# Optimization experiments

Measured on AMD Instinct MI355X. Metric: run time of the kernel, lower is better.

Reference implementation:

```python
import jax, jax.numpy as jnp
import numpy as np

DIM = 512; NHEAD = 8; DHEAD = 64; INNER = NHEAD * DHEAD
CTX = 1024; NOCT = int(np.ceil(np.log2(CTX))) + 1  # 11
B = 8; SEQ = 256; MEM = 768


def positional_encoding(ctx, num_oct):
    # matches Attention.positional_encoding on coords=arange(ctx).view(ctx,1),
    # start_octave = 1 - num_oct
    coords = jnp.arange(ctx, dtype=jnp.float32)[:, None, None]        # (ctx,1,1)
    octaves = jnp.arange(1 - num_oct, 1, dtype=jnp.float32)           # (num_oct,)
    mult = (2.0 ** octaves) * np.pi
    scaled = (coords * mult).reshape(ctx, num_oct)                    # (ctx, num_oct)
    return jnp.concatenate([jnp.sin(scaled), jnp.cos(scaled)], axis=-1)  # (ctx, 2*num_oct)


def get_shifts(mem, seq, ctx):
    coords = jnp.arange(mem + seq - 1, -1, -1) - (seq - 1)            # (mem+seq,)
    shifts = coords[None, :] + jnp.arange(seq)[:, None]               # (seq, mem+seq)
    oob = (shifts < 0) | (shifts > ctx - 1)
    bias = jnp.where(oob, -jnp.inf, 0.0).astype(jnp.float32)
    return jnp.clip(shifts, 0, ctx - 1), bias


def setup_inputs() -> dict:
    key = jax.random.key(0)
    ks = jax.random.split(key, 8)
    s = 0.02
    return {
        "x": jax.random.normal(ks[0], (B, SEQ, DIM), jnp.float32),
        "memory": jax.random.normal(ks[1], (B, MEM, DIM), jnp.float32),
        "W_qkv": jax.random.normal(ks[2], (DIM, 3 * INNER), jnp.float32) * s,
        "W_rel": jax.random.normal(ks[3], (2 * NOCT, INNER), jnp.float32) * s,
        "W_out": jax.random.normal(ks[4], (INNER, DIM), jnp.float32) * s,
        "b_out": jnp.zeros((DIM,), jnp.float32),
        "u_emb": jax.random.normal(ks[5], (DHEAD,), jnp.float32),
        "v_emb": jax.random.normal(ks[6], (DHEAD,), jnp.float32),
    }


def reference(x, memory, W_qkv, W_rel, W_out, b_out, u_emb, v_emb):
    b, seq, _ = x.shape
    mem = memory.shape[1]
    total = mem + seq
    scale = DHEAD ** -0.5

    shifts, bias = get_shifts(mem, seq, CTX)                          # (seq,total) each
    R = positional_encoding(CTX, NOCT)                                # (CTX, 2*NOCT)
    kr = (R @ W_rel)[shifts].reshape(seq, total, NHEAD, DHEAD)        # n m h d

    qkv = jnp.concatenate([memory, x], axis=1) @ W_qkv                # (b,total,3*INNER)
    q, k, v = jnp.split(qkv, 3, axis=-1)

    def heads(t):
        return t.reshape(b, total, NHEAD, DHEAD).transpose(0, 2, 1, 3)  # b h m d

    q = heads(q)[:, :, mem:]                                          # b h n d (queries only over x)
    k = heads(k)
    v = heads(v)

    term_a = jnp.einsum('bhnd,bhmd->bhnm', q, k)
    term_b = jnp.einsum('bhnd,nmhd->bhnm', q, kr)
    term_c = jnp.einsum('d,bhmd->bhm', u_emb, k)[:, :, None, :]        # broadcast over n
    term_d = jnp.einsum('d,nmhd->hnm', v_emb, kr)[None]                # broadcast over b

    dots = (term_a + term_b + term_c + term_d) * scale + bias          # banded -inf mask
    attn = jax.nn.softmax(dots, axis=-1)                               # dropout p=0 -> identity
    out = jnp.einsum('bhnm,bhmd->bnhd', attn, v).reshape(b, seq, INNER)
    return out @ W_out + b_out
```

## Files before the change

### kernel.cpp

```cpp
#include <hip/hip_runtime.h>
#include <hip/hip_bf16.h>
#include <math.h>

typedef unsigned short u16;
typedef unsigned int u32;
typedef __attribute__((ext_vector_type(8))) short short8;
typedef __attribute__((ext_vector_type(4))) float floatx4;

constexpr int kB     = 8;
constexpr int kSEQ   = 256;
constexpr int kMEM   = 768;
constexpr int kTOTAL = 1024;

__device__ __forceinline__ float bf2f(u16 u) {
  return __uint_as_float(((u32)u) << 16);
}
__device__ __forceinline__ u16 f2bf(float f) {
  __hip_bfloat16 h = __float2bfloat16(f);
  return *reinterpret_cast<u16*>(&h);
}
__device__ __forceinline__ void gload_lds16(const u16* g, u16* l) {
  __builtin_amdgcn_global_load_lds(
      (__attribute__((address_space(1))) const unsigned int*)g,
      (__attribute__((address_space(3))) unsigned int*)l, 16, 0, 0);
}

__device__ __forceinline__ void wtconv_body(
    const float* __restrict__ W, u16* __restrict__ Wt, int K, int N,
    int n0, int k0, int tid, float (*tile)[65])
{
  int r = tid >> 4, c4 = (tid & 15) * 4;
#pragma unroll
  for (int v = 0; v < 4; v++) {
    float4 w4 = *(const float4*)(W + (size_t)(k0 + v * 16 + r) * N + n0 + c4);
    tile[v * 16 + r][c4 + 0] = w4.x;
    tile[v * 16 + r][c4 + 1] = w4.y;
    tile[v * 16 + r][c4 + 2] = w4.z;
    tile[v * 16 + r][c4 + 3] = w4.w;
  }
  __syncthreads();
#pragma unroll
  for (int v = 0; v < 4; v++) {
    int rn = v * 16 + r;
    ushort4 o;
    o.x = f2bf(tile[c4 + 0][rn]);
    o.y = f2bf(tile[c4 + 1][rn]);
    o.z = f2bf(tile[c4 + 2][rn]);
    o.w = f2bf(tile[c4 + 3][rn]);
    *(ushort4*)(Wt + (size_t)(n0 + rn) * K + k0 + c4) = o;
  }
}

__global__ __launch_bounds__(256) void prep_kernel(
    const float* __restrict__ x, const float* __restrict__ memf,
    const float* __restrict__ W_qkv, const float* __restrict__ W_out,
    const float* __restrict__ W_rel, const float* __restrict__ v_emb,
    u16* __restrict__ Xb, u16* __restrict__ WqkvT, u16* __restrict__ WoutT,
    u16* __restrict__ Rrel_bf, float* __restrict__ vR)
{
  __shared__ float tile[64][65];
  __shared__ float pe[22];
  __shared__ float prod[512];
  int bid = blockIdx.x;
  int t = threadIdx.x;
  if (bid < 1024) {
    int s = bid;
    if (t < 22) {
      int o = (t < 11) ? t : (t - 11);
      float mult = ldexpf(3.14159265358979323846f, o - 10);
      float ang = (float)s * mult;
      pe[t] = (t < 11) ? sinf(ang) : cosf(ang);
    }
    __syncthreads();
#pragma unroll
    for (int c = 0; c < 2; c++) {
      int j = t + c * 256;
      float acc = 0.f;
#pragma unroll
      for (int o = 0; o < 22; ++o) acc += pe[o] * W_rel[o * 512 + j];
      Rrel_bf[(size_t)s * 512 + j] = f2bf(acc);
      prod[j] = acc * v_emb[j & 63];
    }
    __syncthreads();
    if (t < 8) {
      float a = 0.f;
#pragma unroll 8
      for (int d = 0; d < 64; d++) a += prod[t * 64 + d];
      vR[t * 1024 + s] = a * 0.125f;
    }
  } else if (bid < 3072) {
    int idx = (bid - 1024) * 256 + t;
    int row = idx >> 6, c8 = idx & 63;
    int b = row >> 10, pos = row & 1023;
    const float* src = (pos < kMEM)
        ? memf + (size_t)(b * kMEM + pos) * 512
        : x    + (size_t)(b * kSEQ + pos - kMEM) * 512;
    const float4* s4 = (const float4*)(src + c8 * 8);
    float4 a = s4[0], bb = s4[1];
    u16 tmp[8] = {f2bf(a.x),  f2bf(a.y),  f2bf(a.z),  f2bf(a.w),
                  f2bf(bb.x), f2bf(bb.y), f2bf(bb.z), f2bf(bb.w)};
    *(uint4*)(Xb + (size_t)row * 512 + c8 * 8) = *(uint4*)tmp;
  } else if (bid < 3264) {
    int r = bid - 3072;
    wtconv_body(W_qkv, WqkvT, 512, 1536, (r % 24) * 64, (r / 24) * 64, t, tile);
  } else {
    int r = bid - 3264;
    wtconv_body(W_out, WoutT, 512, 512, (r % 8) * 64, (r / 8) * 64, t, tile);
  }
}

__global__ __launch_bounds__(256) void gemm_bf16(
    const u16* __restrict__ A, const u16* __restrict__ Bt,
    int lda, int ldb, int ksteps,
    u16* __restrict__ Cbf, int ldc, int qscale)
{
  __shared__ u16 As[128 * 64];
  __shared__ u16 Bs[128 * 64];
  int tid = threadIdx.x;
  int id = blockIdx.y * gridDim.x + blockIdx.x;
  int gy = gridDim.y;
  int bm = (id % gy) * 128, bn = (id / gy) * 128;
  int ln = tid & 15, quad = (tid >> 4) & 3, w = tid >> 6;
  int moff = (w >> 1) * 64, noff = (w & 1) * 64;
  int l7 = ln & 7;
  floatx4 acc[4][4];
#pragma unroll
  for (int mi = 0; mi < 4; mi++)
#pragma unroll
    for (int ni = 0; ni < 4; ni++) acc[mi][ni] = (floatx4){0.f, 0.f, 0.f, 0.f};

  int srow[4], sgch[4];
#pragma unroll
  for (int v = 0; v < 4; v++) {
    int f = v * 256 + tid;
    srow[v] = f >> 3;
    sgch[v] = (f & 7) ^ ((f >> 3) & 7);
  }

  for (int ks = 0; ks < ksteps; ks++) {
    int k0 = ks * 64;
#pragma unroll
    for (int v = 0; v < 4; v++) {
      gload_lds16(A + (size_t)(bm + srow[v]) * lda + k0 + sgch[v] * 8,
                  &As[(v * 256 + tid) * 8]);
      gload_lds16(Bt + (size_t)(bn + srow[v]) * ldb + k0 + sgch[v] * 8,
                  &Bs[(v * 256 + tid) * 8]);
    }
    __syncthreads();
#pragma unroll
    for (int kb = 0; kb < 2; kb++) {
      short8 af[4], bfr[4];
#pragma unroll
      for (int mi = 0; mi < 4; mi++) {
        int row = moff + mi * 16 + ln;
        af[mi] = *(const short8*)&As[row * 64 + (((quad + 4 * kb) ^ l7) << 3)];
      }
#pragma unroll
      for (int ni = 0; ni < 4; ni++) {
        int row = noff + ni * 16 + ln;
        bfr[ni] = *(const short8*)&Bs[row * 64 + (((quad + 4 * kb) ^ l7) << 3)];
      }
#pragma unroll
      for (int mi = 0; mi < 4; mi++)
#pragma unroll
        for (int ni = 0; ni < 4; ni++)
          acc[mi][ni] = __builtin_amdgcn_mfma_f32_16x16x32_bf16(
              af[mi], bfr[ni], acc[mi][ni], 0, 0, 0);
    }
    __syncthreads();
  }

  int r0 = bm + moff + quad * 4;
#pragma unroll
  for (int ni = 0; ni < 4; ni++) {
    int col = bn + noff + ni * 16 + ln;
    float scale = (qscale && col < 512) ? 0.125f : 1.f;
#pragma unroll
    for (int mi = 0; mi < 4; mi++) {
#pragma unroll
      for (int r = 0; r < 4; r++) {
        int row = r0 + mi * 16 + r;
        Cbf[(size_t)row * ldc + col] = f2bf(acc[mi][ni][r] * scale);
      }
    }
  }
}

__global__ __launch_bounds__(256) void gemm_bf16_64(
    const u16* __restrict__ A, const u16* __restrict__ Bt,
    int lda, int ldb, int ksteps,
    float* __restrict__ Cf, int ldc, const float* __restrict__ bias)
{
  __shared__ u16 As[64 * 64];
  __shared__ u16 Bs[64 * 64];
  int tid = threadIdx.x;
  int id = blockIdx.y * gridDim.x + blockIdx.x;
  int gy = gridDim.y;
  int bm = (id % gy) * 64, bn = (id / gy) * 64;
  int ln = tid & 15, quad = (tid >> 4) & 3, w = tid >> 6;
  int moff = (w >> 1) * 32, noff = (w & 1) * 32;
  int l7 = ln & 7;
  floatx4 acc[2][2];
#pragma unroll
  for (int mi = 0; mi < 2; mi++)
#pragma unroll
    for (int ni = 0; ni < 2; ni++) acc[mi][ni] = (floatx4){0.f, 0.f, 0.f, 0.f};

  int srow[2], sgch[2];
#pragma unroll
  for (int v = 0; v < 2; v++) {
    int f = v * 256 + tid;
    srow[v] = f >> 3;
    sgch[v] = (f & 7) ^ ((f >> 3) & 7);
  }

  for (int ks = 0; ks < ksteps; ks++) {
    int k0 = ks * 64;
#pragma unroll
    for (int v = 0; v < 2; v++) {
      gload_lds16(A + (size_t)(bm + srow[v]) * lda + k0 + sgch[v] * 8,
                  &As[(v * 256 + tid) * 8]);
      gload_lds16(Bt + (size_t)(bn + srow[v]) * ldb + k0 + sgch[v] * 8,
                  &Bs[(v * 256 + tid) * 8]);
    }
    __syncthreads();
#pragma unroll
    for (int kb = 0; kb < 2; kb++) {
      short8 af[2], bfr[2];
#pragma unroll
      for (int mi = 0; mi < 2; mi++) {
        int row = moff + mi * 16 + ln;
        af[mi] = *(const short8*)&As[row * 64 + (((quad + 4 * kb) ^ l7) << 3)];
      }
#pragma unroll
      for (int ni = 0; ni < 2; ni++) {
        int row = noff + ni * 16 + ln;
        bfr[ni] = *(const short8*)&Bs[row * 64 + (((quad + 4 * kb) ^ l7) << 3)];
      }
#pragma unroll
      for (int mi = 0; mi < 2; mi++)
#pragma unroll
        for (int ni = 0; ni < 2; ni++)
          acc[mi][ni] = __builtin_amdgcn_mfma_f32_16x16x32_bf16(
              af[mi], bfr[ni], acc[mi][ni], 0, 0, 0);
    }
    __syncthreads();
  }

  int r0 = bm + moff + quad * 4;
#pragma unroll
  for (int ni = 0; ni < 2; ni++) {
    int col = bn + noff + ni * 16 + ln;
    float cv = bias[col];
#pragma unroll
    for (int mi = 0; mi < 2; mi++) {
#pragma unroll
      for (int r = 0; r < 4; r++) {
        int row = r0 + mi * 16 + r;
        Cf[(size_t)row * ldc + col] = acc[mi][ni][r] + cv;
      }
    }
  }
}

__global__ __launch_bounds__(256) void attn_mfma(
    const u16* __restrict__ qkv_bf, const u16* __restrict__ Rrel_bf,
    const float* __restrict__ vR, const float* __restrict__ u_emb,
    u16* __restrict__ Opart, float* __restrict__ lbuf)
{
  constexpr int LD  = 72;
  constexpr int TLD = 84;
  __shared__ u16 Vt[2][64 * LD];
  __shared__ u16 Ps[64 * LD];
  __shared__ u16 Tl[4 * 16 * TLD];

  int nt = blockIdx.x >> 3, p = blockIdx.x & 7;
  int h = blockIdx.y, b = blockIdx.z;
  int n0 = nt * 64, bh = b * 8 + h;
  int tid = threadIdx.x;
  int w = tid >> 6, lane = tid & 63;
  int l15 = lane & 15, quad = lane >> 4, q8 = quad * 8;

  int sr0 = tid >> 3, sc8 = tid & 7;
  int sr1 = (256 + tid) >> 3;
  int vg0 = ((sr0 >> 3) ^ sc8) * 8 + (sr0 & 7);
  int vg1 = ((sr1 >> 3) ^ sc8) * 8 + (sr1 & 7);

  const u16* qrow = qkv_bf + (size_t)(b * kTOTAL + kMEM + n0 + 16 * w + l15) * 1536 + h * 64;
  short8 qf0 = *(const short8*)(qrow + q8);
  short8 qf1 = *(const short8*)(qrow + 32 + q8);

  short8 uf0, uf1;
  {
    u16 t0[8], t1[8];
#pragma unroll
    for (int j = 0; j < 8; j++) {
      t0[j] = f2bf(0.125f * u_emb[q8 + j]);
      t1[j] = f2bf(0.125f * u_emb[32 + q8 + j]);
    }
    uf0 = *(short8*)t0;
    uf1 = *(short8*)t1;
  }

  const u16* kpart = qkv_bf + (size_t)(b * kTOTAL) * 1536 + 512 + h * 64;
  const float* vRh = vR + h * 1024;
  u16* Tw = Tl + w * 16 * TLD;

  int ntiles = 13 + nt;
  int mtA = p, mtB = p + 8;
  bool hasB = (mtB < ntiles);
  bool lastB = (mtB == ntiles - 1);

  {
    const u16* va = kpart + (size_t)mtA * 64 * 1536 + 512;
    const u16* vb = kpart + (size_t)mtB * 64 * 1536 + 512;
    uint4 a0 = *(const uint4*)(va + (size_t)sr0 * 1536 + sc8 * 8);
    uint4 a1 = *(const uint4*)(va + (size_t)sr1 * 1536 + sc8 * 8);
    uint4 b0 = *(const uint4*)(vb + (size_t)sr0 * 1536 + sc8 * 8);
    uint4 b1 = *(const uint4*)(vb + (size_t)sr1 * 1536 + sc8 * 8);
    const u16* pa0v = (const u16*)&a0;
    const u16* pa1v = (const u16*)&a1;
    const u16* pb0v = (const u16*)&b0;
    const u16* pb1v = (const u16*)&b1;
#pragma unroll
    for (int i = 0; i < 8; i++) {
      Vt[0][(sc8 * 8 + i) * LD + vg0] = pa0v[i];
      Vt[0][(sc8 * 8 + i) * LD + vg1] = pa1v[i];
      Vt[1][(sc8 * 8 + i) * LD + vg0] = pb0v[i];
      Vt[1][(sc8 * 8 + i) * LD + vg1] = pb1v[i];
    }
  }
  __syncthreads();

  floatx4 o_acc[4];
  float l_i[4];
#pragma unroll
  for (int r = 0; r < 4; r++) l_i[r] = 0.f;
#pragma unroll
  for (int nd = 0; nd < 4; nd++) o_acc[nd] = (floatx4){0.f, 0.f, 0.f, 0.f};

  int s_base_w = kMEM + n0 + 16 * w;

  auto tile_body = [&](int mt, bool lastt, const u16* VtX) {
    int m0 = mt * 64;
    const u16* kbase = kpart + (size_t)m0 * 1536;
    int sb = s_base_w - m0;

    short8 kb0[4], kb1[4];
#pragma unroll
    for (int ni = 0; ni < 4; ni++) {
      const u16* kr = kbase + (size_t)(16 * ni + l15) * 1536;
      kb0[ni] = *(const short8*)(kr + q8);
      kb1[ni] = *(const short8*)(kr + 32 + q8);
    }
    short8 rb0[5], rb1[5];
    float vRc[5];
#pragma unroll
    for (int ct = 0; ct < 5; ct++) {
      int s = sb - 63 + 16 * ct + l15;
      s = min(max(s, 0), 1023);
      const u16* rr = Rrel_bf + (size_t)s * 512 + h * 64;
      rb0[ct] = *(const short8*)(rr + q8);
      rb1[ct] = *(const short8*)(rr + 32 + q8);
      vRc[ct] = vRh[s];
    }

    floatx4 uku[4];
#pragma unroll
    for (int ni = 0; ni < 4; ni++) {
      floatx4 ua = (floatx4){0.f, 0.f, 0.f, 0.f};
      ua = __builtin_amdgcn_mfma_f32_16x16x32_bf16(uf0, kb0[ni], ua, 0, 0, 0);
      ua = __builtin_amdgcn_mfma_f32_16x16x32_bf16(uf1, kb1[ni], ua, 0, 0, 0);
      uku[ni] = ua;
    }

#pragma unroll
    for (int ct = 0; ct < 5; ct++) {
      floatx4 t = (floatx4){0.f, 0.f, 0.f, 0.f};
      t = __builtin_amdgcn_mfma_f32_16x16x32_bf16(qf0, rb0[ct], t, 0, 0, 0);
      t = __builtin_amdgcn_mfma_f32_16x16x32_bf16(qf1, rb1[ct], t, 0, 0, 0);
#pragma unroll
      for (int r = 0; r < 4; r++)
        Tw[(4 * quad + r) * TLD + 16 * ct + l15] = f2bf(t[r] + vRc[ct]);
    }

    floatx4 s_acc[4];
#pragma unroll
    for (int ni = 0; ni < 4; ni++) {
      floatx4 sa = (floatx4){0.f, 0.f, 0.f, 0.f};
      sa = __builtin_amdgcn_mfma_f32_16x16x32_bf16(qf0, kb0[ni], sa, 0, 0, 0);
      sa = __builtin_amdgcn_mfma_f32_16x16x32_bf16(qf1, kb1[ni], sa, 0, 0, 0);
      s_acc[ni] = sa;
    }

#pragma unroll
    for (int r = 0; r < 4; r++) {
      int il = 4 * quad + r;
      float ls = 0.f;
      float pv[4];
#pragma unroll
      for (int ni = 0; ni < 4; ni++) {
        float tsh = bf2f(Tw[il * TLD + 63 + il - 16 * ni - l15]);
        float val = s_acc[ni][r] + tsh + uku[ni][r];
        if (lastt && (16 * ni + l15) > (16 * w + il)) val = -1e30f;
        float e = __expf(val);
        pv[ni] = e;
        ls += e;
      }
      l_i[r] += ls;
      int prow = 16 * w + il;
      int rr3p = prow >> 3;
      int base = prow * LD + (l15 & 7);
#pragma unroll
      for (int ni = 0; ni < 4; ni++)
        Ps[base + (((2 * ni + (l15 >> 3)) ^ rr3p) << 3)] = f2bf(pv[ni]);
    }

    int rowq = 16 * w + l15, rr3q = rowq >> 3;
    short8 pa0 = *(const short8*)&Ps[rowq * LD + ((quad ^ rr3q) << 3)];
    short8 pa1 = *(const short8*)&Ps[rowq * LD + (((quad + 4) ^ rr3q) << 3)];
#pragma unroll
    for (int nd = 0; nd < 4; nd++) {
      int rowv = 16 * nd + l15, rr3v = rowv >> 3;
      short8 vb0 = *(const short8*)&VtX[rowv * LD + ((quad ^ rr3v) << 3)];
      short8 vb1 = *(const short8*)&VtX[rowv * LD + (((quad + 4) ^ rr3v) << 3)];
      o_acc[nd] = __builtin_amdgcn_mfma_f32_16x16x32_bf16(pa0, vb0, o_acc[nd], 0, 0, 0);
      o_acc[nd] = __builtin_amdgcn_mfma_f32_16x16x32_bf16(pa1, vb1, o_acc[nd], 0, 0, 0);
    }
  };

  tile_body(mtA, false, Vt[0]);
  if (hasB) tile_body(mtB, lastB, Vt[1]);

  int pbase = (p * 64 + bh) * 256;
#pragma unroll
  for (int r = 0; r < 4; r++) {
    float l = l_i[r];
#pragma unroll
    for (int off = 1; off < 16; off <<= 1)
      l += __shfl_xor(l, off, 64);
    int n = n0 + 16 * w + 4 * quad + r;
    u16* orow = Opart + ((size_t)(pbase + n) << 6) + l15;
#pragma unroll
    for (int nd = 0; nd < 4; nd++)
      orow[16 * nd] = f2bf(o_acc[nd][r]);
    if (l15 == 0) lbuf[pbase + n] = l;
  }
}

__global__ __launch_bounds__(256) void attn_combine(
    const u16* __restrict__ Opart, const float* __restrict__ lbuf,
    u16* __restrict__ aout_bf)
{
  int idx = blockIdx.x * 256 + threadIdx.x;
  int bh = idx >> 12, n = (idx >> 4) & 255, d4 = idx & 15;
  int rowi = bh * 256 + n;
  float den = 0.f;
  float num[4] = {0.f, 0.f, 0.f, 0.f};
#pragma unroll
  for (int p = 0; p < 8; p++) {
    den += lbuf[(p << 14) + rowi];
    uint2 raw = *(const uint2*)(Opart + (((size_t)(p << 14) + rowi) << 6) + d4 * 4);
    const u16* us = (const u16*)&raw;
#pragma unroll
    for (int j = 0; j < 4; j++) num[j] += bf2f(us[j]);
  }
  float inv = 1.f / den;
  int b = bh >> 3, h = bh & 7;
  ushort4 o;
  o.x = f2bf(num[0] * inv);
  o.y = f2bf(num[1] * inv);
  o.z = f2bf(num[2] * inv);
  o.w = f2bf(num[3] * inv);
  *(ushort4*)(aout_bf + (size_t)(b * kSEQ + n) * 512 + h * 64 + d4 * 4) = o;
}

extern "C" void kernel_launch(void* const* d_in, const int* in_sizes, int n_in,
                              void* d_out, int out_size, void* d_ws, size_t ws_size,
                              hipStream_t stream) {
  (void)in_sizes; (void)n_in; (void)out_size; (void)ws_size;
  const float* x      = (const float*)d_in[0];
  const float* memory = (const float*)d_in[1];
  const float* W_qkv  = (const float*)d_in[2];
  const float* W_rel  = (const float*)d_in[3];
  const float* W_out  = (const float*)d_in[4];
  const float* b_out  = (const float*)d_in[5];
  const float* u_emb  = (const float*)d_in[6];
  const float* v_emb  = (const float*)d_in[7];
  float* out = (float*)d_out;

  char* ws = (char*)d_ws;
  u16*   qkv_bf  = (u16*)ws;                         ws += (size_t)12582912 * 2;
  u16*   Xcat_bf = (u16*)ws;                         ws += (size_t)4194304 * 2;
  u16*   aout_bf = (u16*)ws;                         ws += (size_t)1048576 * 2;
  u16*   Opart   = (u16*)ws;                         ws += (size_t)8388608 * 2;
  float* lbuf    = (float*)ws;                       ws += (size_t)131072 * 4;
  u16*   WqkvT   = (u16*)ws;                         ws += (size_t)786432 * 2;
  u16*   WoutT   = (u16*)ws;                         ws += (size_t)262144 * 2;
  u16*   Rrel_bf = (u16*)ws;                         ws += (size_t)524288 * 2;
  float* vR      = (float*)ws;                       ws += (size_t)8192 * 4;

  prep_kernel<<<3328, 256, 0, stream>>>(
      x, memory, W_qkv, W_out, W_rel, v_emb, Xcat_bf, WqkvT, WoutT, Rrel_bf, vR);

  gemm_bf16<<<dim3(12, 64), 256, 0, stream>>>(
      Xcat_bf, WqkvT, 512, 512, 8, qkv_bf, 1536, 1);

  attn_mfma<<<dim3(32, 8, 8), 256, 0, stream>>>(
      qkv_bf, Rrel_bf, vR, u_emb, Opart, lbuf);

  attn_combine<<<1024, 256, 0, stream>>>(Opart, lbuf, aout_bf);

  gemm_bf16_64<<<dim3(8, 32), 256, 0, stream>>>(
      aout_bf, WoutT, 512, 512, 8, out, 512, b_out);
}
```

Before: 159.2 us.

## Replace LDS relative-shift staging with ds_bpermute and cut attention register pressure

The relative-position term is no longer written to a per-wave LDS tile as bf16 and read back shifted. Each lane now pulls its shifted value straight from registers with ds_bpermute, which also keeps the term in fp32. The u·k bias keeps only one scalar per column block, and the bf16-converted u vector is precomputed once in the prep kernel instead of in every block. Launch bounds ask for 5 waves per SIMD to raise occupancy, at the risk of register spills and extra bpermute traffic.

```diff
diff --git a/kernel.cpp b/kernel.cpp
--- a/kernel.cpp
+++ b/kernel.cpp
@@ -55,8 +55,9 @@
     const float* __restrict__ x, const float* __restrict__ memf,
     const float* __restrict__ W_qkv, const float* __restrict__ W_out,
     const float* __restrict__ W_rel, const float* __restrict__ v_emb,
+    const float* __restrict__ u_emb,
     u16* __restrict__ Xb, u16* __restrict__ WqkvT, u16* __restrict__ WoutT,
-    u16* __restrict__ Rrel_bf, float* __restrict__ vR)
+    u16* __restrict__ Rrel_bf, float* __restrict__ vR, u16* __restrict__ u_bf)
 {
   __shared__ float tile[64][65];
   __shared__ float pe[22];
@@ -65,6 +66,9 @@
   int t = threadIdx.x;
   if (bid < 1024) {
     int s = bid;
+    if (bid == 0 && t >= 128 && t < 192) {
+      u_bf[t - 128] = f2bf(0.125f * u_emb[t - 128]);
+    }
     if (t < 22) {
       int o = (t < 11) ? t : (t - 11);
       float mult = ldexpf(3.14159265358979323846f, o - 10);
@@ -263,16 +267,14 @@
   }
 }
 
-__global__ __launch_bounds__(256) void attn_mfma(
+__global__ __launch_bounds__(256, 5) void attn_mfma(
     const u16* __restrict__ qkv_bf, const u16* __restrict__ Rrel_bf,
-    const float* __restrict__ vR, const float* __restrict__ u_emb,
+    const float* __restrict__ vR, const u16* __restrict__ u_bf,
     u16* __restrict__ Opart, float* __restrict__ lbuf)
 {
-  constexpr int LD  = 72;
-  constexpr int TLD = 84;
+  constexpr int LD = 72;
   __shared__ u16 Vt[2][64 * LD];
   __shared__ u16 Ps[64 * LD];
-  __shared__ u16 Tl[4 * 16 * TLD];
 
   int nt = blockIdx.x >> 3, p = blockIdx.x & 7;
   int h = blockIdx.y, b = blockIdx.z;
@@ -290,21 +292,15 @@
   short8 qf0 = *(const short8*)(qrow + q8);
   short8 qf1 = *(const short8*)(qrow + 32 + q8);
 
-  short8 uf0, uf1;
-  {
-    u16 t0[8], t1[8];
-#pragma unroll
-    for (int j = 0; j < 8; j++) {
-      t0[j] = f2bf(0.125f * u_emb[q8 + j]);
-      t1[j] = f2bf(0.125f * u_emb[32 + q8 + j]);
-    }
-    uf0 = *(short8*)t0;
-    uf1 = *(short8*)t1;
+  int bidx[4];
+#pragma unroll
+  for (int r = 0; r < 4; r++) {
+    int il = 4 * quad + r;
+    bidx[r] = ((quad << 4) | ((il + 15 - l15) & 15)) << 2;
   }
 
   const u16* kpart = qkv_bf + (size_t)(b * kTOTAL) * 1536 + 512 + h * 64;
   const float* vRh = vR + h * 1024;
-  u16* Tw = Tl + w * 16 * TLD;
 
   int ntiles = 13 + nt;
   int mtA = p, mtB = p + 8;
@@ -353,67 +349,55 @@
       kb0[ni] = *(const short8*)(kr + q8);
       kb1[ni] = *(const short8*)(kr + 32 + q8);
     }
-    short8 rb0[5], rb1[5];
-    float vRc[5];
+
+    float uk[4];
+    {
+      short8 uf0 = *(const short8*)(u_bf + q8);
+      short8 uf1 = *(const short8*)(u_bf + 32 + q8);
+#pragma unroll
+      for (int ni = 0; ni < 4; ni++) {
+        floatx4 ua = (floatx4){0.f, 0.f, 0.f, 0.f};
+        ua = __builtin_amdgcn_mfma_f32_16x16x32_bf16(uf0, kb0[ni], ua, 0, 0, 0);
+        ua = __builtin_amdgcn_mfma_f32_16x16x32_bf16(uf1, kb1[ni], ua, 0, 0, 0);
+        uk[ni] = ua[0];
+      }
+    }
+
+    float tf[5][4];
 #pragma unroll
     for (int ct = 0; ct < 5; ct++) {
       int s = sb - 63 + 16 * ct + l15;
       s = min(max(s, 0), 1023);
       const u16* rr = Rrel_bf + (size_t)s * 512 + h * 64;
-      rb0[ct] = *(const short8*)(rr + q8);
-      rb1[ct] = *(const short8*)(rr + 32 + q8);
-      vRc[ct] = vRh[s];
-    }
-
-    floatx4 uku[4];
-#pragma unroll
-    for (int ni = 0; ni < 4; ni++) {
-      floatx4 ua = (floatx4){0.f, 0.f, 0.f, 0.f};
-      ua = __builtin_amdgcn_mfma_f32_16x16x32_bf16(uf0, kb0[ni], ua, 0, 0, 0);
-      ua = __builtin_amdgcn_mfma_f32_16x16x32_bf16(uf1, kb1[ni], ua, 0, 0, 0);
-      uku[ni] = ua;
-    }
-
-#pragma unroll
-    for (int ct = 0; ct < 5; ct++) {
+      short8 rb0 = *(const short8*)(rr + q8);
+      short8 rb1 = *(const short8*)(rr + 32 + q8);
+      float vv = vRh[s];
       floatx4 t = (floatx4){0.f, 0.f, 0.f, 0.f};
-      t = __builtin_amdgcn_mfma_f32_16x16x32_bf16(qf0, rb0[ct], t, 0, 0, 0);
-      t = __builtin_amdgcn_mfma_f32_16x16x32_bf16(qf1, rb1[ct], t, 0, 0, 0);
-#pragma unroll
-      for (int r = 0; r < 4; r++)
-        Tw[(4 * quad + r) * TLD + 16 * ct + l15] = f2bf(t[r] + vRc[ct]);
-    }
-
-    floatx4 s_acc[4];
+      t = __builtin_amdgcn_mfma_f32_16x16x32_bf16(qf0, rb0, t, 0, 0, 0);
+      t = __builtin_amdgcn_mfma_f32_16x16x32_bf16(qf1, rb1, t, 0, 0, 0);
+#pragma unroll
+      for (int r = 0; r < 4; r++) tf[ct][r] = t[r] + vv;
+    }
+
 #pragma unroll
     for (int ni = 0; ni < 4; ni++) {
       floatx4 sa = (floatx4){0.f, 0.f, 0.f, 0.f};
       sa = __builtin_amdgcn_mfma_f32_16x16x32_bf16(qf0, kb0[ni], sa, 0, 0, 0);
       sa = __builtin_amdgcn_mfma_f32_16x16x32_bf16(qf1, kb1[ni], sa, 0, 0, 0);
-      s_acc[ni] = sa;
-    }
-
-#pragma unroll
-    for (int r = 0; r < 4; r++) {
-      int il = 4 * quad + r;
-      float ls = 0.f;
-      float pv[4];
-#pragma unroll
-      for (int ni = 0; ni < 4; ni++) {
-        float tsh = bf2f(Tw[il * TLD + 63 + il - 16 * ni - l15]);
-        float val = s_acc[ni][r] + tsh + uku[ni][r];
+#pragma unroll
+      for (int r = 0; r < 4; r++) {
+        int il = 4 * quad + r;
+        float tv = (l15 < il) ? tf[4 - ni][r] : tf[3 - ni][r];
+        float tsh = __int_as_float(
+            __builtin_amdgcn_ds_bpermute(bidx[r], __float_as_int(tv)));
+        float val = sa[r] + tsh + uk[ni];
         if (lastt && (16 * ni + l15) > (16 * w + il)) val = -1e30f;
         float e = __expf(val);
-        pv[ni] = e;
-        ls += e;
-      }
-      l_i[r] += ls;
-      int prow = 16 * w + il;
-      int rr3p = prow >> 3;
-      int base = prow * LD + (l15 & 7);
-#pragma unroll
-      for (int ni = 0; ni < 4; ni++)
-        Ps[base + (((2 * ni + (l15 >> 3)) ^ rr3p) << 3)] = f2bf(pv[ni]);
+        l_i[r] += e;
+        int prow = 16 * w + il;
+        Ps[prow * LD + (l15 & 7) + (((2 * ni + (l15 >> 3)) ^ (prow >> 3)) << 3)] =
+            f2bf(e);
+      }
     }
 
     int rowq = 16 * w + l15, rr3q = rowq >> 3;
@@ -499,15 +483,17 @@
   u16*   WoutT   = (u16*)ws;                         ws += (size_t)262144 * 2;
   u16*   Rrel_bf = (u16*)ws;                         ws += (size_t)524288 * 2;
   float* vR      = (float*)ws;                       ws += (size_t)8192 * 4;
+  u16*   u_bf    = (u16*)ws;                         ws += (size_t)128;
 
   prep_kernel<<<3328, 256, 0, stream>>>(
-      x, memory, W_qkv, W_out, W_rel, v_emb, Xcat_bf, WqkvT, WoutT, Rrel_bf, vR);
+      x, memory, W_qkv, W_out, W_rel, v_emb, u_emb,
+      Xcat_bf, WqkvT, WoutT, Rrel_bf, vR, u_bf);
 
   gemm_bf16<<<dim3(12, 64), 256, 0, stream>>>(
       Xcat_bf, WqkvT, 512, 512, 8, qkv_bf, 1536, 1);
 
   attn_mfma<<<dim3(32, 8, 8), 256, 0, stream>>>(
-      qkv_bf, Rrel_bf, vR, u_emb, Opart, lbuf);
+      qkv_bf, Rrel_bf, vR, u_bf, Opart, lbuf);
 
   attn_combine<<<1024, 256, 0, stream>>>(Opart, lbuf, aout_bf);
 
```

Measured after the change: 191.2 us. 1.2x slower.
